# Kernel optimization log

Hardware: AMD Instinct MI355X
Metric: run time of the kernel (lower is better)

Reference implementation:

```python
import math
import jax, jax.numpy as jnp
import numpy as np

D_MODEL = 256
NUM_FEATURES = 512  # 2 * d_model (module default)
BATCH, SEQ = 4, 4096
EPS = 1e-6
INPUT_SCALE = 0.25  # keeps exp(xW/sqrt(d) - ||x||^2/2) numerically meaningful


def _make_projection(key):
    # Orthogonal random features: ceil(M/d)=2 QR blocks, then sqrt(|gauss|) row scaling.
    k1, k2, k3 = jax.random.split(key, 3)
    q1, _ = jnp.linalg.qr(jax.random.normal(k1, (D_MODEL, D_MODEL), jnp.float32))
    q2, _ = jnp.linalg.qr(jax.random.normal(k2, (D_MODEL, D_MODEL), jnp.float32))
    proj = jnp.concatenate([q1, q2], axis=1)[:, :NUM_FEATURES]  # (d, M)
    scaling = jnp.sqrt(jnp.abs(jax.random.normal(k3, (D_MODEL, 1), jnp.float32)))
    return proj * scaling


def setup_inputs() -> dict:
    key = jax.random.key(0)
    kq, kk, kv, kp = jax.random.split(key, 4)
    shape = (BATCH, SEQ, D_MODEL)
    return {
        "query": jax.random.normal(kq, shape, jnp.float32) * INPUT_SCALE,
        "key": jax.random.normal(kk, shape, jnp.float32) * INPUT_SCALE,
        "value": jax.random.normal(kv, shape, jnp.float32) * INPUT_SCALE,
        "projection": _make_projection(kp),  # (d_model, num_features) buffer
    }


def _phi(x, projection):
    # phi(x) = exp(xW/sqrt(d) - ||x||^2/2) / sqrt(M)
    d = x.shape[-1]
    m = projection.shape[-1]
    proj = jnp.matmul(x, projection) / math.sqrt(d)  # (B, L, M)
    sq = 0.5 * jnp.sum(x * x, axis=-1, keepdims=True)  # (B, L, 1)
    return jnp.exp(proj - sq) / math.sqrt(m)


def reference(query, key, value, projection):
    qp = _phi(query, projection)  # (B, L, M)
    kp = _phi(key, projection)    # (B, L, M)
    B, L, M = qp.shape
    D = value.shape[-1]

    # Causal linear attention: running KV-state scan, O(B*M*D) state
    # (same math as cumsum of k' (outer) v, without materializing (B,L,M,D)).
    def step(carry, inp):
        kv_state, k_state = carry  # (B,M,D), (B,M)
        q_t, k_t, v_t = inp        # (B,M), (B,M), (B,D)
        kv_state = kv_state + k_t[:, :, None] * v_t[:, None, :]
        k_state = k_state + k_t
        num = jnp.einsum('bm,bmd->bd', q_t, kv_state)
        den = jnp.einsum('bm,bm->b', q_t, k_state)[:, None] + EPS
        return (kv_state, k_state), num / den

    init = (jnp.zeros((B, M, D), qp.dtype), jnp.zeros((B, M), qp.dtype))
    xs = (jnp.swapaxes(qp, 0, 1), jnp.swapaxes(kp, 0, 1), jnp.swapaxes(value, 0, 1))
    _, out = jax.lax.scan(step, init, xs)  # (L, B, D)
    return jnp.swapaxes(out, 0, 1)  # (B, L, D)
```

## Files before the change

kernel.cpp:

```cpp
#include <hip/hip_runtime.h>

#define B_ 4
#define L_ 4096
#define D_ 256
#define M_ 512
#define C_ 256
#define NC_ 16
#define NG_ (B_*NC_)
#define EPS_ 1e-6f
#define RSQRT_D_ 0.0625f
#define RSQRT_M_ 0.044194173824159216f

typedef __attribute__((ext_vector_type(8))) short short8;
typedef __attribute__((ext_vector_type(4))) short short4v;
typedef __attribute__((ext_vector_type(4))) float floatx4;

__device__ __forceinline__ short f2b(float f) {
  union { float f; unsigned u; } c; c.f = f;
  unsigned r = c.u + 0x7fffu + ((c.u >> 16) & 1u);
  return (short)(r >> 16);
}
__device__ __forceinline__ float b2f(short s) {
  union { unsigned u; float f; } c; c.u = ((unsigned)(unsigned short)s) << 16;
  return c.f;
}

#define OFF_S    0u
#define OFF_WT   33554432u
#define OFF_QP   41943040u
#undef OFF_WT
#undef OFF_QP
#define OFF_WT   67108864u
#define OFF_QP   67371008u
#define OFF_KP   84148224u
#define OFF_KPT  100925440u
#define OFF_VT   117702656u
#undef OFF_WT
#undef OFF_QP
#undef OFF_KP
#undef OFF_KPT
#undef OFF_VT
#define OFF_SB   0u
#define OFF_SB2  0u
#define OFF_WT2  16777216u
#define OFF_QP2  17039360u
#define OFF_KP2  33816576u
#define OFF_KPT2 50593792u
#define OFF_VT2  67371008u
#define OFF_AM2  75759616u
#define OFF_PB2  84148224u
#define OFF_ZP2  84148224u
#define OFF_Z2   100925440u
#define OFF_DEN2 101056512u

__device__ __forceinline__ void mfma_tile_gemm(
    const short* __restrict__ Ag, int lda,
    const short* __restrict__ Bg, int ldb,
    int K, short* sA, short* sB, floatx4 acc[4][4])
{
  const int tid  = threadIdx.x;
  const int lane = tid & 63;
  const int wave = tid >> 6;
  const int wm = wave >> 1, wn = wave & 1;
  const int q = lane >> 4, ml = lane & 15;

  short8 pa[4], pb[4];
  #pragma unroll
  for (int it = 0; it < 4; ++it) {
    int ci = tid + 256 * it;
    int m = ci >> 3, k8 = ci & 7;
    pa[it] = *(const short8*)(Ag + (size_t)m * lda + k8 * 8);
    pb[it] = *(const short8*)(Bg + (size_t)m * ldb + k8 * 8);
  }
  for (int k0 = 0; k0 < K; k0 += 64) {
    #pragma unroll
    for (int it = 0; it < 4; ++it) {
      int ci = tid + 256 * it;
      int m = ci >> 3, k8 = ci & 7;
      int dst = (k8 >> 2) * 512 + (m >> 4) * 64 + (k8 & 3) * 16 + ((m & 15) ^ k8);
      *(short8*)(sA + dst * 8) = pa[it];
      *(short8*)(sB + dst * 8) = pb[it];
    }
    if (k0 + 64 < K) {
      #pragma unroll
      for (int it = 0; it < 4; ++it) {
        int ci = tid + 256 * it;
        int m = ci >> 3, k8 = ci & 7;
        pa[it] = *(const short8*)(Ag + (size_t)m * lda + k0 + 64 + k8 * 8);
        pb[it] = *(const short8*)(Bg + (size_t)m * ldb + k0 + 64 + k8 * 8);
      }
    }
    __syncthreads();
    #pragma unroll
    for (int ks = 0; ks < 2; ++ks) {
      short8 a[4], b[4];
      int k8 = ks * 4 + q;
      #pragma unroll
      for (int i = 0; i < 4; ++i) {
        int ca = ks * 512 + (wm * 4 + i) * 64 + q * 16 + (ml ^ k8);
        a[i] = *(const short8*)(sA + ca * 8);
        int cb = ks * 512 + (wn * 4 + i) * 64 + q * 16 + (ml ^ k8);
        b[i] = *(const short8*)(sB + cb * 8);
      }
      #pragma unroll
      for (int i = 0; i < 4; ++i)
        #pragma unroll
        for (int j = 0; j < 4; ++j)
          acc[i][j] = __builtin_amdgcn_mfma_f32_16x16x32_bf16(a[i], b[j], acc[i][j], 0, 0, 0);
    }
    __syncthreads();
  }
}

__global__ __launch_bounds__(256) void transpose_cvt_kernel(
    const float* __restrict__ v, const float* __restrict__ W,
    short* __restrict__ vT, short* __restrict__ Wt)
{
  const int z = blockIdx.z;
  const float* src; short* dst; int ld_in, ld_out;
  if (z < NG_) {
    if (blockIdx.x >= 4) return;
    src = v + (size_t)z * (C_*D_) + (size_t)blockIdx.y * 64 * D_ + blockIdx.x * 64;
    dst = vT + (size_t)z * (D_*C_) + (size_t)blockIdx.x * 64 * C_ + blockIdx.y * 64;
    ld_in = D_; ld_out = C_;
  } else {
    src = W + (size_t)blockIdx.y * 64 * M_ + blockIdx.x * 64;
    dst = Wt + (size_t)blockIdx.x * 64 * D_ + blockIdx.y * 64;
    ld_in = M_; ld_out = D_;
  }
  __shared__ short sm[64 * 65];
  const int tid = threadIdx.x;
  #pragma unroll
  for (int it = 0; it < 4; ++it) {
    int ci = tid + 256 * it;
    int row = ci >> 4, c4 = ci & 15;
    float4 x = *(const float4*)(src + (size_t)row * ld_in + c4 * 4);
    sm[(c4 * 4 + 0) * 65 + row] = f2b(x.x);
    sm[(c4 * 4 + 1) * 65 + row] = f2b(x.y);
    sm[(c4 * 4 + 2) * 65 + row] = f2b(x.z);
    sm[(c4 * 4 + 3) * 65 + row] = f2b(x.w);
  }
  __syncthreads();
  #pragma unroll
  for (int it = 0; it < 2; ++it) {
    int ci = tid + 256 * it;
    int dr = ci >> 3, t8 = ci & 7;
    short8 o;
    #pragma unroll
    for (int u = 0; u < 8; ++u) o[u] = sm[dr * 65 + t8 * 8 + u];
    *(short8*)(dst + (size_t)dr * ld_out + t8 * 8) = o;
  }
}

__global__ __launch_bounds__(256) void phi_mfma_kernel(
    const float* __restrict__ qin, const float* __restrict__ kin,
    const short* __restrict__ Wt,
    short* __restrict__ qp, short* __restrict__ kp, short* __restrict__ kpT)
{
  const bool is_k = (blockIdx.z == 1);
  const float* X = is_k ? kin : qin;
  short* outP = is_k ? kp : qp;
  const int id = blockIdx.x + 4 * blockIdx.y;
  const int row0 = ((id & 7) + 8 * (id >> 5)) * 128;
  const int col0 = ((id >> 3) & 3) * 128;
  __shared__ short smem[17664];
  short* sA = smem;
  short* sB = smem + 8192;
  float* sqs = (float*)(smem + 17408);
  const int tid = threadIdx.x, lane = tid & 63, wave = tid >> 6;
  const int wm = wave >> 1, wn = wave & 1, q = lane >> 4, ml = lane & 15;
  floatx4 acc[4][4];
  #pragma unroll
  for (int i = 0; i < 4; ++i)
    #pragma unroll
    for (int j = 0; j < 4; ++j) acc[i][j] = (floatx4){0.f,0.f,0.f,0.f};

  float4 px0[4], px1[4];
  #pragma unroll
  for (int it = 0; it < 4; ++it) {
    int ci = tid + 256 * it;
    int m = ci >> 3, c = ci & 7;
    const float* src = X + (size_t)(row0 + m) * D_ + c * 8;
    px0[it] = *(const float4*)src;
    px1[it] = *(const float4*)(src + 4);
  }
  float ssq[4] = {0.f, 0.f, 0.f, 0.f};
  for (int k0 = 0; k0 < D_; k0 += 64) {
    #pragma unroll
    for (int it = 0; it < 4; ++it) {
      int ci = tid + 256 * it;
      int m = ci >> 3, c = ci & 7;
      short8 wb = *(const short8*)(Wt + (size_t)(col0 + m) * D_ + k0 + c * 8);
      float4 x0 = px0[it], x1 = px1[it];
      short8 vv;
      vv[0] = f2b(x0.x); vv[1] = f2b(x0.y); vv[2] = f2b(x0.z); vv[3] = f2b(x0.w);
      vv[4] = f2b(x1.x); vv[5] = f2b(x1.y); vv[6] = f2b(x1.z); vv[7] = f2b(x1.w);
      ssq[it] += x0.x*x0.x + x0.y*x0.y + x0.z*x0.z + x0.w*x0.w
               + x1.x*x1.x + x1.y*x1.y + x1.z*x1.z + x1.w*x1.w;
      *(short8*)(sA + (c * 128 + (m ^ c)) * 8) = vv;
      *(short8*)(sB + (c * 128 + (m ^ c)) * 8) = wb;
    }
    if (k0 + 64 < D_) {
      #pragma unroll
      for (int it = 0; it < 4; ++it) {
        int ci = tid + 256 * it;
        int m = ci >> 3, c = ci & 7;
        const float* src = X + (size_t)(row0 + m) * D_ + k0 + 64 + c * 8;
        px0[it] = *(const float4*)src;
        px1[it] = *(const float4*)(src + 4);
      }
    }
    __syncthreads();
    #pragma unroll
    for (int ks = 0; ks < 2; ++ks) {
      short8 a[4], b[4];
      int c = ks * 4 + q;
      #pragma unroll
      for (int i = 0; i < 4; ++i) {
        int ra = (wm * 64 + i * 16 + ml) ^ c;
        a[i] = *(const short8*)(sA + (c * 128 + ra) * 8);
        int rb = (wn * 64 + i * 16 + ml) ^ c;
        b[i] = *(const short8*)(sB + (c * 128 + rb) * 8);
      }
      #pragma unroll
      for (int i = 0; i < 4; ++i)
        #pragma unroll
        for (int j = 0; j < 4; ++j)
          acc[i][j] = __builtin_amdgcn_mfma_f32_16x16x32_bf16(a[i], b[j], acc[i][j], 0, 0, 0);
    }
    __syncthreads();
  }
  #pragma unroll
  for (int o = 1; o < 8; o <<= 1)
    #pragma unroll
    for (int it = 0; it < 4; ++it) ssq[it] += __shfl_xor(ssq[it], o);
  if ((tid & 7) == 0) {
    #pragma unroll
    for (int it = 0; it < 4; ++it) sqs[(tid >> 3) + 32 * it] = 0.5f * ssq[it];
  }
  __syncthreads();
  #pragma unroll
  for (int i = 0; i < 4; ++i) {
    int rl = wm * 64 + i * 16 + q * 4;
    float sqv[4];
    #pragma unroll
    for (int r = 0; r < 4; ++r) sqv[r] = sqs[rl + r];
    #pragma unroll
    for (int j = 0; j < 4; ++j) {
      int cl = wn * 64 + j * 16 + ml;
      short4v tb;
      #pragma unroll
      for (int r = 0; r < 4; ++r) {
        float pv = __expf(fmaf(acc[i][j][r], RSQRT_D_, -sqv[r])) * RSQRT_M_;
        short bv = f2b(pv);
        outP[(size_t)(row0 + rl + r) * M_ + col0 + cl] = bv;
        tb[r] = bv;
      }
      if (is_k)
        *(short4v*)(smem + (size_t)cl * 136 + rl) = tb;
    }
  }
  if (is_k) {
    __syncthreads();
    int g = row0 >> 8, tb0 = row0 & 255;
    #pragma unroll
    for (int it = 0; it < 8; ++it) {
      int ci = tid + 256 * it;
      int t8 = ci & 15, cc = ci >> 4;
      short8 vv = *(const short8*)(smem + (size_t)cc * 136 + t8 * 8);
      *(short8*)(kpT + (size_t)g * (M_*C_) + (size_t)(col0 + cc) * C_ + tb0 + t8 * 8) = vv;
    }
  }
}

__global__ __launch_bounds__(256) void mega_kernel(
    const short* __restrict__ vT, const short* __restrict__ kpT,
    const short* __restrict__ qp, const short* __restrict__ kp,
    short* __restrict__ Sb, short* __restrict__ Am, float* __restrict__ ZP)
{
  const int id = blockIdx.x + 4 * blockIdx.y + 16 * blockIdx.z;
  const int g  = (id & 7) + 8 * (id >> 7);
  const int inner = (id >> 3) & 15;
  const int bx = inner & 3, by = inner >> 2;
  __shared__ short smem[16384];
  const int tid = threadIdx.x;

  if (by == 3) {
    const int mb = bx & 1, p = bx >> 1;
    if (p >= 2) return;
    const int m = mb * 256 + tid;
    const short* base = kp + ((size_t)g * C_ + p * 128) * M_ + m;
    float s = 0.f;
    #pragma unroll 8
    for (int t = 0; t < 128; ++t) s += b2f(base[(size_t)t * M_]);
    ZP[((size_t)g * 2 + p) * M_ + m] = s;
    return;
  }

  floatx4 acc[4][4];
  #pragma unroll
  for (int i = 0; i < 4; ++i)
    #pragma unroll
    for (int j = 0; j < 4; ++j) acc[i][j] = (floatx4){0.f,0.f,0.f,0.f};
  const int lane = tid & 63, wave = tid >> 6;
  const int wm = wave >> 1, wn = wave & 1, q = lane >> 4, ln = lane & 15;

  if (by < 2) {
    const int m0 = bx * 128, d0 = by * 128;
    mfma_tile_gemm(vT + (size_t)g * (D_*C_) + (size_t)d0 * C_, C_,
                   kpT + (size_t)g * (M_*C_) + (size_t)m0 * C_, C_, C_,
                   smem, smem + 8192, acc);
    #pragma unroll
    for (int i = 0; i < 4; ++i) {
      int rl = d0 + wm * 64 + i * 16 + q * 4;
      #pragma unroll
      for (int j = 0; j < 4; ++j) {
        int cl = m0 + wn * 64 + j * 16 + ln;
        #pragma unroll
        for (int r = 0; r < 4; ++r)
          Sb[((size_t)g * D_ + rl + r) * M_ + cl] = f2b(acc[i][j][r]);
      }
    }
  } else {
    const int tt0 = (bx >> 1) * 128, tp0 = (bx & 1) * 128;
    short* Ag = Am + (size_t)g * (C_*C_);
    if (tp0 > tt0) {
      short8 z8 = 0;
      #pragma unroll
      for (int it = 0; it < 8; ++it) {
        int ci = tid + 256 * it;
        int row = ci >> 4, c8 = ci & 15;
        *(short8*)(Ag + (size_t)(tt0 + row) * C_ + tp0 + c8 * 8) = z8;
      }
      return;
    }
    const size_t cb = (size_t)g * C_;
    mfma_tile_gemm(qp + (cb + tt0) * M_, M_, kp + (cb + tp0) * M_, M_, M_,
                   smem, smem + 8192, acc);
    #pragma unroll
    for (int i = 0; i < 4; ++i) {
      int rl = tt0 + wm * 64 + i * 16 + q * 4;
      #pragma unroll
      for (int j = 0; j < 4; ++j) {
        int cl = tp0 + wn * 64 + j * 16 + ln;
        #pragma unroll
        for (int r = 0; r < 4; ++r) {
          short bv = (cl <= rl + r) ? f2b(acc[i][j][r]) : (short)0;
          Ag[(size_t)(rl + r) * C_ + cl] = bv;
        }
      }
    }
  }
}

__global__ __launch_bounds__(256) void prefixz_kernel(
    const float* __restrict__ ZP, float* __restrict__ z)
{
  int j = blockIdx.x * 256 + threadIdx.x;
  int b = j >> 9, m = j & 511;
  float run = 0.f;
  for (int i = 0; i < NC_; ++i) {
    int g = b * NC_ + i;
    z[(size_t)g * M_ + m] = run;
    const float* zp = ZP + (size_t)g * 2 * M_ + m;
    run += zp[0] + zp[M_];
  }
}

__global__ __launch_bounds__(256) void prefixS_kernel(
    const short* __restrict__ Sb, short* __restrict__ Pb)
{
  int j = blockIdx.x * 256 + threadIdx.x;
  int b = j >> 17, e = j & 131071;
  float run = 0.f;
  size_t idx = ((size_t)b * NC_) * 131072 + e;
  for (int i = 0; i < NC_; ++i) {
    float t = b2f(Sb[idx]);
    Pb[idx] = f2b(run);
    run += t;
    idx += 131072;
  }
}

__global__ __launch_bounds__(256) void den_kernel(
    const short* __restrict__ qp, const float* __restrict__ z,
    const short* __restrict__ Am, float* __restrict__ den)
{
  int wid  = blockIdx.x * 4 + (threadIdx.x >> 6);
  int lane = threadIdx.x & 63;
  int g = wid >> 8, tl = wid & 255;
  short8 qv = *(const short8*)(qp + (size_t)wid * M_ + lane * 8);
  const float* zp = z + (size_t)g * M_ + lane * 8;
  float4 z1 = *(const float4*)(zp);
  float4 z2 = *(const float4*)(zp + 4);
  float s = 0.f;
  s = fmaf(b2f(qv[0]), z1.x, s); s = fmaf(b2f(qv[1]), z1.y, s);
  s = fmaf(b2f(qv[2]), z1.z, s); s = fmaf(b2f(qv[3]), z1.w, s);
  s = fmaf(b2f(qv[4]), z2.x, s); s = fmaf(b2f(qv[5]), z2.y, s);
  s = fmaf(b2f(qv[6]), z2.z, s); s = fmaf(b2f(qv[7]), z2.w, s);
  short4v av = *(const short4v*)(Am + (size_t)g * (C_*C_) + (size_t)tl * C_ + lane * 4);
  s += b2f(av.x) + b2f(av.y) + b2f(av.z) + b2f(av.w);
  #pragma unroll
  for (int off = 32; off > 0; off >>= 1) s += __shfl_down(s, off);
  if (lane == 0) den[wid] = s + EPS_;
}

__global__ __launch_bounds__(256) void out_mfma_kernel(
    const short* __restrict__ qp, const short* __restrict__ Pb,
    const short* __restrict__ Am, const short* __restrict__ vT,
    const float* __restrict__ den, float* __restrict__ out)
{
  const int id = blockIdx.x + 2 * blockIdx.y + 4 * blockIdx.z;
  const int g  = (id & 7) + 8 * (id >> 5);
  const int inner = (id >> 3) & 3;
  const int d0 = (inner & 1) * 128, tt0 = (inner >> 1) * 128;
  __shared__ short smem[16384];
  floatx4 acc[4][4];
  #pragma unroll
  for (int i = 0; i < 4; ++i)
    #pragma unroll
    for (int j = 0; j < 4; ++j) acc[i][j] = (floatx4){0.f,0.f,0.f,0.f};
  mfma_tile_gemm(qp + ((size_t)g * C_ + tt0) * M_, M_,
                 Pb + (size_t)g * (D_*M_) + (size_t)d0 * M_, M_, M_,
                 smem, smem + 8192, acc);
  mfma_tile_gemm(Am + ((size_t)g * C_ + tt0) * C_, C_,
                 vT + (size_t)g * (D_*C_) + (size_t)d0 * C_, C_, C_,
                 smem, smem + 8192, acc);
  const int tid = threadIdx.x, lane = tid & 63, wave = tid >> 6;
  const int wm = wave >> 1, wn = wave & 1, q = lane >> 4, ln = lane & 15;
  #pragma unroll
  for (int i = 0; i < 4; ++i) {
    int rl = tt0 + wm * 64 + i * 16 + q * 4;
    #pragma unroll
    for (int r = 0; r < 4; ++r) {
      int grow = g * C_ + rl + r;
      float rc = 1.0f / den[grow];
      #pragma unroll
      for (int j = 0; j < 4; ++j) {
        int cl = d0 + wn * 64 + j * 16 + ln;
        out[(size_t)grow * D_ + cl] = acc[i][j][r] * rc;
      }
    }
  }
}

extern "C" void kernel_launch(void* const* d_in, const int* in_sizes, int n_in,
                              void* d_out, int out_size, void* d_ws, size_t ws_size,
                              hipStream_t stream) {
  const float* q = (const float*)d_in[0];
  const float* k = (const float*)d_in[1];
  const float* v = (const float*)d_in[2];
  const float* W = (const float*)d_in[3];
  float* out = (float*)d_out;
  char* ws = (char*)d_ws;

  short* Sb  = (short*)(ws + OFF_SB2);
  short* Wt  = (short*)(ws + OFF_WT2);
  short* qp  = (short*)(ws + OFF_QP2);
  short* kp  = (short*)(ws + OFF_KP2);
  short* kpT = (short*)(ws + OFF_KPT2);
  short* vT  = (short*)(ws + OFF_VT2);
  short* Am  = (short*)(ws + OFF_AM2);
  short* Pb  = (short*)(ws + OFF_PB2);
  float* ZP  = (float*)(ws + OFF_ZP2);
  float* z   = (float*)(ws + OFF_Z2);
  float* den = (float*)(ws + OFF_DEN2);

  transpose_cvt_kernel<<<dim3(8, 4, NG_ + 1), 256, 0, stream>>>(v, W, vT, Wt);
  phi_mfma_kernel<<<dim3(M_/128, (B_*L_)/128, 2), 256, 0, stream>>>(q, k, Wt, qp, kp, kpT);
  mega_kernel<<<dim3(4, 4, NG_), 256, 0, stream>>>(vT, kpT, qp, kp, Sb, Am, ZP);
  prefixz_kernel<<<8, 256, 0, stream>>>(ZP, z);
  prefixS_kernel<<<(B_*D_*M_)/256, 256, 0, stream>>>(Sb, Pb);
  den_kernel<<<(B_*L_)/4, 256, 0, stream>>>(qp, z, Am, den);
  out_mfma_kernel<<<dim3(D_/128, C_/128, NG_), 256, 0, stream>>>(qp, Pb, Am, vT, den, out);
}
```

Measured before the change: 165.8 us.

## Fuse z-prefix and denominator computation into output GEMM kernel

Removes the separate prefixz and den kernels. The output kernel now computes the per-chunk z prefix into shared memory, and accumulates the denominator from the A-tiles it already loads for both GEMMs (q·z and row sums of the masked A). This saves two launches and the extra global reads of qp and Am. In exchange, each block redundantly sums up to 15 ZP rows, and the GEMM loader does extra per-element FMA work. The workspace layout macros are also cleaned up.

Result: faster. 161.3 us (-2.8%).

```diff
diff --git a/kernel.cpp b/kernel.cpp
--- a/kernel.cpp
+++ b/kernel.cpp
@@ -25,33 +25,15 @@
   return c.f;
 }
 
-#define OFF_S    0u
-#define OFF_WT   33554432u
-#define OFF_QP   41943040u
-#undef OFF_WT
-#undef OFF_QP
-#define OFF_WT   67108864u
-#define OFF_QP   67371008u
-#define OFF_KP   84148224u
-#define OFF_KPT  100925440u
-#define OFF_VT   117702656u
-#undef OFF_WT
-#undef OFF_QP
-#undef OFF_KP
-#undef OFF_KPT
-#undef OFF_VT
 #define OFF_SB   0u
-#define OFF_SB2  0u
-#define OFF_WT2  16777216u
-#define OFF_QP2  17039360u
-#define OFF_KP2  33816576u
-#define OFF_KPT2 50593792u
-#define OFF_VT2  67371008u
-#define OFF_AM2  75759616u
-#define OFF_PB2  84148224u
-#define OFF_ZP2  84148224u
-#define OFF_Z2   100925440u
-#define OFF_DEN2 101056512u
+#define OFF_WT   16777216u
+#define OFF_QP   17039360u
+#define OFF_KP   33816576u
+#define OFF_KPT  50593792u
+#define OFF_VT   67371008u
+#define OFF_AM   75759616u
+#define OFF_PB   84148224u
+#define OFF_ZP   100925440u
 
 __device__ __forceinline__ void mfma_tile_gemm(
     const short* __restrict__ Ag, int lda,
@@ -353,20 +335,6 @@
   }
 }
 
-__global__ __launch_bounds__(256) void prefixz_kernel(
-    const float* __restrict__ ZP, float* __restrict__ z)
-{
-  int j = blockIdx.x * 256 + threadIdx.x;
-  int b = j >> 9, m = j & 511;
-  float run = 0.f;
-  for (int i = 0; i < NC_; ++i) {
-    int g = b * NC_ + i;
-    z[(size_t)g * M_ + m] = run;
-    const float* zp = ZP + (size_t)g * 2 * M_ + m;
-    run += zp[0] + zp[M_];
-  }
-}
-
 __global__ __launch_bounds__(256) void prefixS_kernel(
     const short* __restrict__ Sb, short* __restrict__ Pb)
 {
@@ -382,62 +350,183 @@
   }
 }
 
-__global__ __launch_bounds__(256) void den_kernel(
-    const short* __restrict__ qp, const float* __restrict__ z,
-    const short* __restrict__ Am, float* __restrict__ den)
-{
-  int wid  = blockIdx.x * 4 + (threadIdx.x >> 6);
-  int lane = threadIdx.x & 63;
-  int g = wid >> 8, tl = wid & 255;
-  short8 qv = *(const short8*)(qp + (size_t)wid * M_ + lane * 8);
-  const float* zp = z + (size_t)g * M_ + lane * 8;
-  float4 z1 = *(const float4*)(zp);
-  float4 z2 = *(const float4*)(zp + 4);
-  float s = 0.f;
-  s = fmaf(b2f(qv[0]), z1.x, s); s = fmaf(b2f(qv[1]), z1.y, s);
-  s = fmaf(b2f(qv[2]), z1.z, s); s = fmaf(b2f(qv[3]), z1.w, s);
-  s = fmaf(b2f(qv[4]), z2.x, s); s = fmaf(b2f(qv[5]), z2.y, s);
-  s = fmaf(b2f(qv[6]), z2.z, s); s = fmaf(b2f(qv[7]), z2.w, s);
-  short4v av = *(const short4v*)(Am + (size_t)g * (C_*C_) + (size_t)tl * C_ + lane * 4);
-  s += b2f(av.x) + b2f(av.y) + b2f(av.z) + b2f(av.w);
-  #pragma unroll
-  for (int off = 32; off > 0; off >>= 1) s += __shfl_down(s, off);
-  if (lane == 0) den[wid] = s + EPS_;
-}
-
 __global__ __launch_bounds__(256) void out_mfma_kernel(
     const short* __restrict__ qp, const short* __restrict__ Pb,
     const short* __restrict__ Am, const short* __restrict__ vT,
-    const float* __restrict__ den, float* __restrict__ out)
+    const float* __restrict__ ZP, float* __restrict__ out)
 {
   const int id = blockIdx.x + 2 * blockIdx.y + 4 * blockIdx.z;
   const int g  = (id & 7) + 8 * (id >> 5);
   const int inner = (id >> 3) & 3;
   const int d0 = (inner & 1) * 128, tt0 = (inner >> 1) * 128;
   __shared__ short smem[16384];
+  __shared__ float zbuf[512];
+  __shared__ float dbuf[128];
+  short* sA = smem; short* sB = smem + 8192;
+  const int tid = threadIdx.x, lane = tid & 63, wave = tid >> 6;
+  const int wm = wave >> 1, wn = wave & 1, q = lane >> 4, ml = lane & 15;
+  const int r8 = tid >> 3;
+
+  {
+    int b = g >> 4, gi = g & 15;
+    float s0 = 0.f, s1 = 0.f;
+    const float* zp0 = ZP + (size_t)(b * NC_) * 2 * M_;
+    for (int i = 0; i < gi; ++i) {
+      const float* r = zp0 + (size_t)i * 2 * M_;
+      s0 += r[tid] + r[M_ + tid];
+      s1 += r[tid + 256] + r[M_ + tid + 256];
+    }
+    zbuf[tid] = s0; zbuf[tid + 256] = s1;
+    if (tid < 128) dbuf[tid] = 0.f;
+  }
+  __syncthreads();
+
   floatx4 acc[4][4];
   #pragma unroll
   for (int i = 0; i < 4; ++i)
     #pragma unroll
     for (int j = 0; j < 4; ++j) acc[i][j] = (floatx4){0.f,0.f,0.f,0.f};
-  mfma_tile_gemm(qp + ((size_t)g * C_ + tt0) * M_, M_,
-                 Pb + (size_t)g * (D_*M_) + (size_t)d0 * M_, M_, M_,
-                 smem, smem + 8192, acc);
-  mfma_tile_gemm(Am + ((size_t)g * C_ + tt0) * C_, C_,
-                 vT + (size_t)g * (D_*C_) + (size_t)d0 * C_, C_, C_,
-                 smem, smem + 8192, acc);
-  const int tid = threadIdx.x, lane = tid & 63, wave = tid >> 6;
-  const int wm = wave >> 1, wn = wave & 1, q = lane >> 4, ln = lane & 15;
+
+  {
+    const short* Ag = qp + ((size_t)g * C_ + tt0) * M_;
+    const short* Bg = Pb + (size_t)g * (D_*M_) + (size_t)d0 * M_;
+    float dp[4] = {0.f, 0.f, 0.f, 0.f};
+    short8 pa[4], pb[4];
+    #pragma unroll
+    for (int it = 0; it < 4; ++it) {
+      int ci = tid + 256 * it;
+      int m = ci >> 3, k8 = ci & 7;
+      pa[it] = *(const short8*)(Ag + (size_t)m * M_ + k8 * 8);
+      pb[it] = *(const short8*)(Bg + (size_t)m * M_ + k8 * 8);
+    }
+    for (int k0 = 0; k0 < M_; k0 += 64) {
+      #pragma unroll
+      for (int it = 0; it < 4; ++it) {
+        int ci = tid + 256 * it;
+        int m = ci >> 3, k8 = ci & 7;
+        int dst = (k8 >> 2) * 512 + (m >> 4) * 64 + (k8 & 3) * 16 + ((m & 15) ^ k8);
+        *(short8*)(sA + dst * 8) = pa[it];
+        *(short8*)(sB + dst * 8) = pb[it];
+        const float* zz = zbuf + k0 + k8 * 8;
+        float d = 0.f;
+        #pragma unroll
+        for (int u = 0; u < 8; ++u) d = fmaf(b2f(pa[it][u]), zz[u], d);
+        dp[it] += d;
+      }
+      if (k0 + 64 < M_) {
+        #pragma unroll
+        for (int it = 0; it < 4; ++it) {
+          int ci = tid + 256 * it;
+          int m = ci >> 3, k8 = ci & 7;
+          pa[it] = *(const short8*)(Ag + (size_t)m * M_ + k0 + 64 + k8 * 8);
+          pb[it] = *(const short8*)(Bg + (size_t)m * M_ + k0 + 64 + k8 * 8);
+        }
+      }
+      __syncthreads();
+      #pragma unroll
+      for (int ks = 0; ks < 2; ++ks) {
+        short8 a[4], b[4];
+        int k8 = ks * 4 + q;
+        #pragma unroll
+        for (int i = 0; i < 4; ++i) {
+          int ca = ks * 512 + (wm * 4 + i) * 64 + q * 16 + (ml ^ k8);
+          a[i] = *(const short8*)(sA + ca * 8);
+          int cb = ks * 512 + (wn * 4 + i) * 64 + q * 16 + (ml ^ k8);
+          b[i] = *(const short8*)(sB + cb * 8);
+        }
+        #pragma unroll
+        for (int i = 0; i < 4; ++i)
+          #pragma unroll
+          for (int j = 0; j < 4; ++j)
+            acc[i][j] = __builtin_amdgcn_mfma_f32_16x16x32_bf16(a[i], b[j], acc[i][j], 0, 0, 0);
+      }
+      __syncthreads();
+    }
+    #pragma unroll
+    for (int o = 1; o < 8; o <<= 1)
+      #pragma unroll
+      for (int it = 0; it < 4; ++it) dp[it] += __shfl_xor(dp[it], o);
+    if ((tid & 7) == 0) {
+      #pragma unroll
+      for (int it = 0; it < 4; ++it) dbuf[r8 + 32 * it] += dp[it];
+    }
+  }
+
+  {
+    const short* Ag = Am + ((size_t)g * C_ + tt0) * C_;
+    const short* Bg = vT + (size_t)g * (D_*C_) + (size_t)d0 * C_;
+    float dp[4] = {0.f, 0.f, 0.f, 0.f};
+    short8 pa[4], pb[4];
+    #pragma unroll
+    for (int it = 0; it < 4; ++it) {
+      int ci = tid + 256 * it;
+      int m = ci >> 3, k8 = ci & 7;
+      pa[it] = *(const short8*)(Ag + (size_t)m * C_ + k8 * 8);
+      pb[it] = *(const short8*)(Bg + (size_t)m * C_ + k8 * 8);
+    }
+    for (int k0 = 0; k0 < C_; k0 += 64) {
+      #pragma unroll
+      for (int it = 0; it < 4; ++it) {
+        int ci = tid + 256 * it;
+        int m = ci >> 3, k8 = ci & 7;
+        int dst = (k8 >> 2) * 512 + (m >> 4) * 64 + (k8 & 3) * 16 + ((m & 15) ^ k8);
+        *(short8*)(sA + dst * 8) = pa[it];
+        *(short8*)(sB + dst * 8) = pb[it];
+        float d = 0.f;
+        #pragma unroll
+        for (int u = 0; u < 8; ++u) d += b2f(pa[it][u]);
+        dp[it] += d;
+      }
+      if (k0 + 64 < C_) {
+        #pragma unroll
+        for (int it = 0; it < 4; ++it) {
+          int ci = tid + 256 * it;
+          int m = ci >> 3, k8 = ci & 7;
+          pa[it] = *(const short8*)(Ag + (size_t)m * C_ + k0 + 64 + k8 * 8);
+          pb[it] = *(const short8*)(Bg + (size_t)m * C_ + k0 + 64 + k8 * 8);
+        }
+      }
+      __syncthreads();
+      #pragma unroll
+      for (int ks = 0; ks < 2; ++ks) {
+        short8 a[4], b[4];
+        int k8 = ks * 4 + q;
+        #pragma unroll
+        for (int i = 0; i < 4; ++i) {
+          int ca = ks * 512 + (wm * 4 + i) * 64 + q * 16 + (ml ^ k8);
+          a[i] = *(const short8*)(sA + ca * 8);
+          int cb = ks * 512 + (wn * 4 + i) * 64 + q * 16 + (ml ^ k8);
+          b[i] = *(const short8*)(sB + cb * 8);
+        }
+        #pragma unroll
+        for (int i = 0; i < 4; ++i)
+          #pragma unroll
+          for (int j = 0; j < 4; ++j)
+            acc[i][j] = __builtin_amdgcn_mfma_f32_16x16x32_bf16(a[i], b[j], acc[i][j], 0, 0, 0);
+      }
+      __syncthreads();
+    }
+    #pragma unroll
+    for (int o = 1; o < 8; o <<= 1)
+      #pragma unroll
+      for (int it = 0; it < 4; ++it) dp[it] += __shfl_xor(dp[it], o);
+    if ((tid & 7) == 0) {
+      #pragma unroll
+      for (int it = 0; it < 4; ++it) dbuf[r8 + 32 * it] += dp[it];
+    }
+  }
+  __syncthreads();
+
   #pragma unroll
   for (int i = 0; i < 4; ++i) {
-    int rl = tt0 + wm * 64 + i * 16 + q * 4;
+    int lr = wm * 64 + i * 16 + q * 4;
     #pragma unroll
     for (int r = 0; r < 4; ++r) {
-      int grow = g * C_ + rl + r;
-      float rc = 1.0f / den[grow];
+      int grow = g * C_ + tt0 + lr + r;
+      float rc = 1.0f / (dbuf[lr + r] + EPS_);
       #pragma unroll
       for (int j = 0; j < 4; ++j) {
-        int cl = d0 + wn * 64 + j * 16 + ln;
+        int cl = d0 + wn * 64 + j * 16 + ml;
         out[(size_t)grow * D_ + cl] = acc[i][j][r] * rc;
       }
     }
@@ -454,23 +543,19 @@
   float* out = (float*)d_out;
   char* ws = (char*)d_ws;
 
-  short* Sb  = (short*)(ws + OFF_SB2);
-  short* Wt  = (short*)(ws + OFF_WT2);
-  short* qp  = (short*)(ws + OFF_QP2);
-  short* kp  = (short*)(ws + OFF_KP2);
-  short* kpT = (short*)(ws + OFF_KPT2);
-  short* vT  = (short*)(ws + OFF_VT2);
-  short* Am  = (short*)(ws + OFF_AM2);
-  short* Pb  = (short*)(ws + OFF_PB2);
-  float* ZP  = (float*)(ws + OFF_ZP2);
-  float* z   = (float*)(ws + OFF_Z2);
-  float* den = (float*)(ws + OFF_DEN2);
+  short* Sb  = (short*)(ws + OFF_SB);
+  short* Wt  = (short*)(ws + OFF_WT);
+  short* qp  = (short*)(ws + OFF_QP);
+  short* kp  = (short*)(ws + OFF_KP);
+  short* kpT = (short*)(ws + OFF_KPT);
+  short* vT  = (short*)(ws + OFF_VT);
+  short* Am  = (short*)(ws + OFF_AM);
+  short* Pb  = (short*)(ws + OFF_PB);
+  float* ZP  = (float*)(ws + OFF_ZP);
 
   transpose_cvt_kernel<<<dim3(8, 4, NG_ + 1), 256, 0, stream>>>(v, W, vT, Wt);
   phi_mfma_kernel<<<dim3(M_/128, (B_*L_)/128, 2), 256, 0, stream>>>(q, k, Wt, qp, kp, kpT);
   mega_kernel<<<dim3(4, 4, NG_), 256, 0, stream>>>(vT, kpT, qp, kp, Sb, Am, ZP);
-  prefixz_kernel<<<8, 256, 0, stream>>>(ZP, z);
   prefixS_kernel<<<(B_*D_*M_)/256, 256, 0, stream>>>(Sb, Pb);
-  den_kernel<<<(B_*L_)/4, 256, 0, stream>>>(qp, z, Am, den);
-  out_mfma_kernel<<<dim3(D_/128, C_/128, NG_), 256, 0, stream>>>(qp, Pb, Am, vT, den, out);
-}
+  out_mfma_kernel<<<dim3(D_/128, C_/128, NG_), 256, 0, stream>>>(qp, Pb, Am, vT, ZP, out);
+}
```
